# Optimization experiments

Measured on AMD Instinct MI355X. Metric: run time of the kernel, lower is better.

Reference implementation:

```python
import jax, jax.numpy as jnp
import numpy as np
from jax import lax

R = 1          # guided filter radius
EPS = 1e-05    # regularizer


def _box_filter(x, r):
    # Separable moving-average, VALID padding (matches Keras DepthwiseConv2D default).
    # Original applies filter_y (k,1) first, then filter_x (1,k).
    k = 2 * r + 1
    c = x.shape[-1]
    ky = jnp.full((k, 1, 1, c), 1.0 / k, x.dtype)  # HWIO depthwise kernel
    kx = jnp.full((1, k, 1, c), 1.0 / k, x.dtype)
    dn = lax.conv_dimension_numbers(x.shape, ky.shape, ('NHWC', 'HWIO', 'NHWC'))
    x = lax.conv_general_dilated(x, ky, (1, 1), 'VALID', dimension_numbers=dn,
                                 feature_group_count=c)
    x = lax.conv_general_dilated(x, kx, (1, 1), 'VALID', dimension_numbers=dn,
                                 feature_group_count=c)
    return x


def setup_inputs() -> dict:
    key = jax.random.key(0)
    k1, k2, k3 = jax.random.split(key, 3)
    lr_x = jax.random.normal(k1, (2, 270, 480, 4), jnp.float32)
    lr_y = jax.random.normal(k2, (2, 270, 480, 4), jnp.float32)
    hr_x = jax.random.normal(k3, (2, 1080, 1920, 4), jnp.float32)
    return {"lr_x": lr_x, "lr_y": lr_y, "hr_x": hr_x}


def reference(lr_x, lr_y, hr_x):
    mean_x = _box_filter(lr_x, R)                              # [B, H-2r, W-2r, C]
    mean_y = _box_filter(lr_y, R)
    cov_xy = _box_filter(lr_x * lr_y, R) - mean_x * mean_y
    var_x = _box_filter(lr_x * lr_x, R) - mean_x * mean_x
    A = cov_xy / (var_x + EPS)
    b = mean_y - A * mean_x
    B, H, W, C = hr_x.shape
    mean_A = jax.image.resize(A, (B, H, W, C), method='bilinear', antialias=False)
    mean_b = jax.image.resize(b, (B, H, W, C), method='bilinear', antialias=False)
    return mean_A * hr_x + mean_b
```

## Files before the change

### kernel.cpp

```cpp
#include <hip/hip_runtime.h>


namespace {

constexpr int LR_H = 270, LR_W = 480;
constexpr int A_H  = 268, A_W  = 478;
constexpr int HR_H = 1080, HR_W = 1920;
constexpr int BATCH = 2;
constexpr float EPS_F = 1e-5f;

constexpr int TILE_W = 240;
constexpr int NTILES = HR_W / TILE_W;
constexpr int ROWS   = 5;
constexpr int ROWGRP = HR_H / ROWS;
constexpr int VCOLS  = 64;
constexpr int ACOLS  = 62;
constexpr int RSETS  = 3;

using f32x4 = __attribute__((ext_vector_type(4))) float;

__device__ __forceinline__ float4 f4add(float4 a, float4 b) {
    return make_float4(a.x + b.x, a.y + b.y, a.z + b.z, a.w + b.w);
}
__device__ __forceinline__ float4 f4sub(float4 a, float4 b) {
    return make_float4(a.x - b.x, a.y - b.y, a.z - b.z, a.w - b.w);
}
__device__ __forceinline__ float4 f4mul(float4 a, float4 b) {
    return make_float4(a.x * b.x, a.y * b.y, a.z * b.z, a.w * b.w);
}
__device__ __forceinline__ float4 f4scale(float4 a, float s) {
    return make_float4(a.x * s, a.y * s, a.z * s, a.w * s);
}
__device__ __forceinline__ float4 f4fma(float4 a, float4 b, float4 c) {
    return make_float4(fmaf(a.x, b.x, c.x), fmaf(a.y, b.y, c.y),
                       fmaf(a.z, b.z, c.z), fmaf(a.w, b.w, c.w));
}
__device__ __forceinline__ float4 f4lerp(float4 a, float4 b, float t) {
    return make_float4(fmaf(t, b.x - a.x, a.x), fmaf(t, b.y - a.y, a.y),
                       fmaf(t, b.z - a.z, a.z), fmaf(t, b.w - a.w, a.w));
}
__device__ __forceinline__ float4 f4axpy(float s, float4 v, float4 acc) {
    return make_float4(fmaf(s, v.x, acc.x), fmaf(s, v.y, acc.y),
                       fmaf(s, v.z, acc.z), fmaf(s, v.w, acc.w));
}
__device__ __forceinline__ float4 f4rcp(float4 a) {
    return make_float4(__builtin_amdgcn_rcpf(a.x), __builtin_amdgcn_rcpf(a.y),
                       __builtin_amdgcn_rcpf(a.z), __builtin_amdgcn_rcpf(a.w));
}
__device__ __forceinline__ void nt_store(float4 v, float4* p) {
    f32x4 rv = {v.x, v.y, v.z, v.w};
    __builtin_nontemporal_store(rv, (f32x4*)p);
}

}

__global__ __launch_bounds__(256) void
fgf_fused5(const float4* __restrict__ lr_x,
           const float4* __restrict__ lr_y,
           const float4* __restrict__ hr_x,
           float4* __restrict__ out) {
    __shared__ float4 vs[RSETS][4][VCOLS];
    __shared__ float4 sA4[RSETS][ACOLS];
    __shared__ float4 sB4[RSETS][ACOLS];

    int bid  = blockIdx.x;
    int tile = bid & (NTILES - 1);
    int g    = bid >> 3;
    int rg   = g % ROWGRP;
    int b    = g / ROWGRP;
    int tid  = threadIdx.x;

    constexpr float sh_scale = (float)A_H / (float)HR_H;
    constexpr float sw_scale = (float)A_W / (float)HR_W;

    int hbase = rg * ROWS;
    int R0 = (int)floorf((hbase + 0.5f) * sh_scale - 0.5f);

    int w_start = tile * TILE_W;
    int c0 = (int)floorf((w_start + 0.5f) * sw_scale - 0.5f);

    int w = w_start + tid;
    bool valid = (tid < TILE_W);
    size_t hr_row0 = ((size_t)b * HR_H + hbase) * (size_t)HR_W + w;
    float4 xr[ROWS];
#pragma unroll
    for (int j = 0; j < ROWS; ++j) {
        xr[j] = valid ? hr_x[hr_row0 + (size_t)j * HR_W]
                      : make_float4(0.f, 0.f, 0.f, 0.f);
    }

    if (tid < RSETS * VCOLS) {
        int rs = tid >> 6;
        int cs = tid & 63;
        int ar = min(max(R0 + rs, 0), A_H - 1);
        int col = min(max(c0 + cs, 0), LR_W - 1);
        const float4* px = lr_x + ((size_t)b * LR_H + ar) * LR_W + col;
        const float4* py = lr_y + ((size_t)b * LR_H + ar) * LR_W + col;
        float4 sx  = make_float4(0.f, 0.f, 0.f, 0.f);
        float4 sy  = make_float4(0.f, 0.f, 0.f, 0.f);
        float4 sxy = make_float4(0.f, 0.f, 0.f, 0.f);
        float4 sxx = make_float4(0.f, 0.f, 0.f, 0.f);
#pragma unroll
        for (int dy = 0; dy < 3; ++dy) {
            float4 x = px[(size_t)dy * LR_W];
            float4 y = py[(size_t)dy * LR_W];
            sx  = f4add(sx, x);
            sy  = f4add(sy, y);
            sxy = f4fma(x, y, sxy);
            sxx = f4fma(x, x, sxx);
        }
        vs[rs][0][cs] = sx;
        vs[rs][1][cs] = sy;
        vs[rs][2][cs] = sxy;
        vs[rs][3][cs] = sxx;
    }
    __syncthreads();

    constexpr float inv9 = 1.0f / 9.0f;
    {
        int rs = tid >> 6;
        int sl = tid & 63;
        if (rs < RSETS && sl < ACOLS) {
            int a  = min(max(c0 + sl, 0), A_W - 1);
            int bs = a - c0;
            float4 hx  = f4add(f4add(vs[rs][0][bs], vs[rs][0][bs + 1]), vs[rs][0][bs + 2]);
            float4 hy  = f4add(f4add(vs[rs][1][bs], vs[rs][1][bs + 1]), vs[rs][1][bs + 2]);
            float4 hxy = f4add(f4add(vs[rs][2][bs], vs[rs][2][bs + 1]), vs[rs][2][bs + 2]);
            float4 hxx = f4add(f4add(vs[rs][3][bs], vs[rs][3][bs + 1]), vs[rs][3][bs + 2]);
            float4 mx  = f4scale(hx, inv9);
            float4 my  = f4scale(hy, inv9);
            float4 cov = f4sub(f4scale(hxy, inv9), f4mul(mx, my));
            float4 var = f4sub(f4scale(hxx, inv9), f4mul(mx, mx));
            float4 A = f4mul(cov, f4rcp(make_float4(var.x + EPS_F, var.y + EPS_F,
                                                    var.z + EPS_F, var.w + EPS_F)));
            float4 bb = f4sub(my, f4mul(A, mx));
            sA4[rs][sl] = A;
            sB4[rs][sl] = bb;
        }
    }
    __syncthreads();

    if (valid) {
        float sw = (w + 0.5f) * sw_scale - 0.5f;
        float fw = floorf(sw);
        float tw = sw - fw;
        int wi = min((int)fw - c0, ACOLS - 2);

        float4 hA0 = f4lerp(sA4[0][wi], sA4[0][wi + 1], tw);
        float4 hB0 = f4lerp(sB4[0][wi], sB4[0][wi + 1], tw);
        float4 hA1 = f4lerp(sA4[1][wi], sA4[1][wi + 1], tw);
        float4 hB1 = f4lerp(sB4[1][wi], sB4[1][wi + 1], tw);
        float4 hA2 = f4lerp(sA4[2][wi], sA4[2][wi + 1], tw);
        float4 hB2 = f4lerp(sB4[2][wi], sB4[2][wi + 1], tw);

#pragma unroll
        for (int j = 0; j < ROWS; ++j) {
            float shj = (hbase + j + 0.5f) * sh_scale - 0.5f;
            float t = shj - (float)R0;
            float w0 = fmaxf(1.f - t, 0.f);
            float w1 = 1.f - fabsf(t - 1.f);
            float w2 = fmaxf(t - 1.f, 0.f);

            float4 aI = f4axpy(w2, hA2, f4axpy(w1, hA1, f4scale(hA0, w0)));
            float4 bI = f4axpy(w2, hB2, f4axpy(w1, hB1, f4scale(hB0, w0)));

            nt_store(f4fma(aI, xr[j], bI), &out[hr_row0 + (size_t)j * HR_W]);
        }
    }
}

extern "C" void kernel_launch(void* const* d_in, const int* in_sizes, int n_in,
                              void* d_out, int out_size, void* d_ws, size_t ws_size,
                              hipStream_t stream) {
    const float4* lr_x = (const float4*)d_in[0];
    const float4* lr_y = (const float4*)d_in[1];
    const float4* hr_x = (const float4*)d_in[2];
    float4* out = (float4*)d_out;

    constexpr int nblocks = BATCH * ROWGRP * NTILES;
    fgf_fused5<<<nblocks, 256, 0, stream>>>(lr_x, lr_y, hr_x, out);
}
```

Baseline: 26.39 us.

## Make each wavefront an independent 64-pixel tile with wave-level barriers

Each 64-lane wave now owns a 64-column by 5-row output tile and computes its own box-filter sums and A/b coefficients in a private slice of shared memory. Block-wide __syncthreads are replaced with wave barriers, and all lanes are active instead of leaving 16 of 256 threads idle. The cost is redundant low-res halo loads and box-filter work across the many narrow tiles, a larger share of lanes doing idle clamped work in the coefficient stage, and reliance on wave-synchronous LDS ordering.

```diff
diff --git a/kernel.cpp b/kernel.cpp
--- a/kernel.cpp
+++ b/kernel.cpp
@@ -9,13 +9,14 @@
 constexpr int BATCH = 2;
 constexpr float EPS_F = 1e-5f;
 
-constexpr int TILE_W = 240;
-constexpr int NTILES = HR_W / TILE_W;
-constexpr int ROWS   = 5;
+constexpr int WTILE = 64;
+constexpr int NWT   = HR_W / WTILE;
+constexpr int ROWS  = 5;
 constexpr int ROWGRP = HR_H / ROWS;
-constexpr int VCOLS  = 64;
-constexpr int ACOLS  = 62;
-constexpr int RSETS  = 3;
+constexpr int RSETS = 3;
+constexpr int WVC   = 20;
+constexpr int WAC   = 18;
+constexpr int WSLOT = RSETS * 4 * WVC;
 
 using f32x4 = __attribute__((ext_vector_type(4))) float;
 
@@ -55,20 +56,21 @@
 }
 
 __global__ __launch_bounds__(256) void
-fgf_fused5(const float4* __restrict__ lr_x,
-           const float4* __restrict__ lr_y,
-           const float4* __restrict__ hr_x,
-           float4* __restrict__ out) {
-    __shared__ float4 vs[RSETS][4][VCOLS];
-    __shared__ float4 sA4[RSETS][ACOLS];
-    __shared__ float4 sB4[RSETS][ACOLS];
+fgf_wave(const float4* __restrict__ lr_x,
+         const float4* __restrict__ lr_y,
+         const float4* __restrict__ hr_x,
+         float4* __restrict__ out) {
+    __shared__ float4 smem[4][WSLOT];
 
-    int bid  = blockIdx.x;
-    int tile = bid & (NTILES - 1);
-    int g    = bid >> 3;
-    int rg   = g % ROWGRP;
-    int b    = g / ROWGRP;
     int tid  = threadIdx.x;
+    int wid  = tid >> 6;
+    int lane = tid & 63;
+    int widx = blockIdx.x * 4 + wid;
+
+    int wt = widx % NWT;
+    int g  = widx / NWT;
+    int rg = g % ROWGRP;
+    int b  = g / ROWGRP;
 
     constexpr float sh_scale = (float)A_H / (float)HR_H;
     constexpr float sw_scale = (float)A_W / (float)HR_W;
@@ -76,96 +78,86 @@
     int hbase = rg * ROWS;
     int R0 = (int)floorf((hbase + 0.5f) * sh_scale - 0.5f);
 
-    int w_start = tile * TILE_W;
-    int c0 = (int)floorf((w_start + 0.5f) * sw_scale - 0.5f);
+    int w0px = wt * WTILE;
+    int c0 = (int)floorf((w0px + 0.5f) * sw_scale - 0.5f);
 
-    int w = w_start + tid;
-    bool valid = (tid < TILE_W);
-    size_t hr_row0 = ((size_t)b * HR_H + hbase) * (size_t)HR_W + w;
+    float4* vs = &smem[wid][0];
+
+    int t = min(lane, RSETS * WVC - 1);
+    int rs = t / WVC;
+    int cs = t - rs * WVC;
+    int ar  = min(max(R0 + rs, 0), A_H - 1);
+    int col = min(max(c0 + cs, 0), LR_W - 1);
+    const float4* px = lr_x + ((size_t)b * LR_H + ar) * LR_W + col;
+    const float4* py = lr_y + ((size_t)b * LR_H + ar) * LR_W + col;
+    float4 x0 = px[0], x1 = px[LR_W], x2 = px[2 * LR_W];
+    float4 y0 = py[0], y1 = py[LR_W], y2 = py[2 * LR_W];
+
+    int w = w0px + lane;
+    size_t hr0 = ((size_t)b * HR_H + hbase) * (size_t)HR_W + w;
     float4 xr[ROWS];
 #pragma unroll
     for (int j = 0; j < ROWS; ++j) {
-        xr[j] = valid ? hr_x[hr_row0 + (size_t)j * HR_W]
-                      : make_float4(0.f, 0.f, 0.f, 0.f);
+        xr[j] = hr_x[hr0 + (size_t)j * HR_W];
     }
 
-    if (tid < RSETS * VCOLS) {
-        int rs = tid >> 6;
-        int cs = tid & 63;
-        int ar = min(max(R0 + rs, 0), A_H - 1);
-        int col = min(max(c0 + cs, 0), LR_W - 1);
-        const float4* px = lr_x + ((size_t)b * LR_H + ar) * LR_W + col;
-        const float4* py = lr_y + ((size_t)b * LR_H + ar) * LR_W + col;
-        float4 sx  = make_float4(0.f, 0.f, 0.f, 0.f);
-        float4 sy  = make_float4(0.f, 0.f, 0.f, 0.f);
-        float4 sxy = make_float4(0.f, 0.f, 0.f, 0.f);
-        float4 sxx = make_float4(0.f, 0.f, 0.f, 0.f);
-#pragma unroll
-        for (int dy = 0; dy < 3; ++dy) {
-            float4 x = px[(size_t)dy * LR_W];
-            float4 y = py[(size_t)dy * LR_W];
-            sx  = f4add(sx, x);
-            sy  = f4add(sy, y);
-            sxy = f4fma(x, y, sxy);
-            sxx = f4fma(x, x, sxx);
-        }
-        vs[rs][0][cs] = sx;
-        vs[rs][1][cs] = sy;
-        vs[rs][2][cs] = sxy;
-        vs[rs][3][cs] = sxx;
-    }
-    __syncthreads();
+    float4 sx  = f4add(f4add(x0, x1), x2);
+    float4 sy  = f4add(f4add(y0, y1), y2);
+    float4 sxy = f4fma(x0, y0, f4fma(x1, y1, f4mul(x2, y2)));
+    float4 sxx = f4fma(x0, x0, f4fma(x1, x1, f4mul(x2, x2)));
+    vs[rs * (4 * WVC) + 0 * WVC + cs] = sx;
+    vs[rs * (4 * WVC) + 1 * WVC + cs] = sy;
+    vs[rs * (4 * WVC) + 2 * WVC + cs] = sxy;
+    vs[rs * (4 * WVC) + 3 * WVC + cs] = sxx;
+    __builtin_amdgcn_wave_barrier();
 
     constexpr float inv9 = 1.0f / 9.0f;
-    {
-        int rs = tid >> 6;
-        int sl = tid & 63;
-        if (rs < RSETS && sl < ACOLS) {
-            int a  = min(max(c0 + sl, 0), A_W - 1);
-            int bs = a - c0;
-            float4 hx  = f4add(f4add(vs[rs][0][bs], vs[rs][0][bs + 1]), vs[rs][0][bs + 2]);
-            float4 hy  = f4add(f4add(vs[rs][1][bs], vs[rs][1][bs + 1]), vs[rs][1][bs + 2]);
-            float4 hxy = f4add(f4add(vs[rs][2][bs], vs[rs][2][bs + 1]), vs[rs][2][bs + 2]);
-            float4 hxx = f4add(f4add(vs[rs][3][bs], vs[rs][3][bs + 1]), vs[rs][3][bs + 2]);
-            float4 mx  = f4scale(hx, inv9);
-            float4 my  = f4scale(hy, inv9);
-            float4 cov = f4sub(f4scale(hxy, inv9), f4mul(mx, my));
-            float4 var = f4sub(f4scale(hxx, inv9), f4mul(mx, mx));
-            float4 A = f4mul(cov, f4rcp(make_float4(var.x + EPS_F, var.y + EPS_F,
-                                                    var.z + EPS_F, var.w + EPS_F)));
-            float4 bb = f4sub(my, f4mul(A, mx));
-            sA4[rs][sl] = A;
-            sB4[rs][sl] = bb;
-        }
-    }
-    __syncthreads();
+    int t2  = min(lane, RSETS * WAC - 1);
+    int rs2 = t2 / WAC;
+    int sl  = t2 - rs2 * WAC;
+    int a   = min(max(c0 + sl, 0), A_W - 1);
+    int bs  = a - c0;
+    const float4* vb = vs + rs2 * (4 * WVC) + bs;
+    float4 hx  = f4add(f4add(vb[0],       vb[1]),           vb[2]);
+    float4 hy  = f4add(f4add(vb[WVC],     vb[WVC + 1]),     vb[WVC + 2]);
+    float4 hxy = f4add(f4add(vb[2 * WVC], vb[2 * WVC + 1]), vb[2 * WVC + 2]);
+    float4 hxx = f4add(f4add(vb[3 * WVC], vb[3 * WVC + 1]), vb[3 * WVC + 2]);
+    float4 mx  = f4scale(hx, inv9);
+    float4 my  = f4scale(hy, inv9);
+    float4 cov = f4sub(f4scale(hxy, inv9), f4mul(mx, my));
+    float4 var = f4sub(f4scale(hxx, inv9), f4mul(mx, mx));
+    float4 A = f4mul(cov, f4rcp(make_float4(var.x + EPS_F, var.y + EPS_F,
+                                            var.z + EPS_F, var.w + EPS_F)));
+    float4 bb = f4sub(my, f4mul(A, mx));
+    __builtin_amdgcn_wave_barrier();
+    vs[(rs2 * 2 + 0) * WAC + sl] = A;
+    vs[(rs2 * 2 + 1) * WAC + sl] = bb;
+    __builtin_amdgcn_wave_barrier();
 
-    if (valid) {
-        float sw = (w + 0.5f) * sw_scale - 0.5f;
-        float fw = floorf(sw);
-        float tw = sw - fw;
-        int wi = min((int)fw - c0, ACOLS - 2);
+    float swf = (w + 0.5f) * sw_scale - 0.5f;
+    float fw = floorf(swf);
+    float tw = swf - fw;
+    int wi = (int)fw - c0;
 
-        float4 hA0 = f4lerp(sA4[0][wi], sA4[0][wi + 1], tw);
-        float4 hB0 = f4lerp(sB4[0][wi], sB4[0][wi + 1], tw);
-        float4 hA1 = f4lerp(sA4[1][wi], sA4[1][wi + 1], tw);
-        float4 hB1 = f4lerp(sB4[1][wi], sB4[1][wi + 1], tw);
-        float4 hA2 = f4lerp(sA4[2][wi], sA4[2][wi + 1], tw);
-        float4 hB2 = f4lerp(sB4[2][wi], sB4[2][wi + 1], tw);
+    float4 hA0 = f4lerp(vs[0 * WAC + wi], vs[0 * WAC + wi + 1], tw);
+    float4 hB0 = f4lerp(vs[1 * WAC + wi], vs[1 * WAC + wi + 1], tw);
+    float4 hA1 = f4lerp(vs[2 * WAC + wi], vs[2 * WAC + wi + 1], tw);
+    float4 hB1 = f4lerp(vs[3 * WAC + wi], vs[3 * WAC + wi + 1], tw);
+    float4 hA2 = f4lerp(vs[4 * WAC + wi], vs[4 * WAC + wi + 1], tw);
+    float4 hB2 = f4lerp(vs[5 * WAC + wi], vs[5 * WAC + wi + 1], tw);
 
 #pragma unroll
-        for (int j = 0; j < ROWS; ++j) {
-            float shj = (hbase + j + 0.5f) * sh_scale - 0.5f;
-            float t = shj - (float)R0;
-            float w0 = fmaxf(1.f - t, 0.f);
-            float w1 = 1.f - fabsf(t - 1.f);
-            float w2 = fmaxf(t - 1.f, 0.f);
+    for (int j = 0; j < ROWS; ++j) {
+        float shj = (hbase + j + 0.5f) * sh_scale - 0.5f;
+        float tv = shj - (float)R0;
+        float w0 = fmaxf(1.f - tv, 0.f);
+        float w1 = 1.f - fabsf(tv - 1.f);
+        float w2 = fmaxf(tv - 1.f, 0.f);
 
-            float4 aI = f4axpy(w2, hA2, f4axpy(w1, hA1, f4scale(hA0, w0)));
-            float4 bI = f4axpy(w2, hB2, f4axpy(w1, hB1, f4scale(hB0, w0)));
+        float4 aI = f4axpy(w2, hA2, f4axpy(w1, hA1, f4scale(hA0, w0)));
+        float4 bI = f4axpy(w2, hB2, f4axpy(w1, hB1, f4scale(hB0, w0)));
 
-            nt_store(f4fma(aI, xr[j], bI), &out[hr_row0 + (size_t)j * HR_W]);
-        }
+        nt_store(f4fma(aI, xr[j], bI), &out[hr0 + (size_t)j * HR_W]);
     }
 }
 
@@ -177,6 +169,6 @@
     const float4* hr_x = (const float4*)d_in[2];
     float4* out = (float4*)d_out;
 
-    constexpr int nblocks = BATCH * ROWGRP * NTILES;
-    fgf_fused5<<<nblocks, 256, 0, stream>>>(lr_x, lr_y, hr_x, out);
+    constexpr int nblocks = BATCH * ROWGRP * NWT / 4;
+    fgf_wave<<<nblocks, 256, 0, stream>>>(lr_x, lr_y, hr_x, out);
 }
```

Result: slower. 28.39 us (+7.6%).
